# Kernel tuning notes

Measured on AMD Instinct MI355X. Metric: run time of the kernel, lower is better.

Reference implementation:

```python
import jax, jax.numpy as jnp
import numpy as np

NF4_LUT = jnp.array([-1.0, -0.6961928009986877, -0.5250730514526367, -0.39491748809814453,
                     -0.28444138169288635, -0.18477343022823334, -0.09105003625154495, 0.0,
                     0.07958029955625534, 0.16093020141124725, 0.24611230194568634,
                     0.33791524171829224, 0.44070982933044434, 0.5626170039176941,
                     0.7229568362236023, 1.0], dtype=jnp.float32)

B, S, IN, OUT, GS = 4, 2048, 4096, 4096, 128


def setup_inputs() -> dict:
    key = jax.random.key(0)
    k1, k2, k3, k4 = jax.random.split(key, 4)
    x = jax.random.normal(k1, (B, S, IN), dtype=jnp.float32)
    # each int32 entry is one packed byte holding two 4-bit NF4 codes (low nibble first)
    qweight = jax.random.randint(k2, (OUT, IN // 2), 0, 256, dtype=jnp.int32)
    scales = jax.random.uniform(k3, (OUT, IN // GS), dtype=jnp.float32, minval=0.01, maxval=0.1)
    bias = jax.random.normal(k4, (OUT,), dtype=jnp.float32)
    g_idx = (jnp.arange(IN, dtype=jnp.int32) // GS).astype(jnp.int32)
    lut = NF4_LUT
    return {"x": x, "qweight": qweight, "scales": scales, "bias": bias,
            "g_idx": g_idx, "lut": lut}


def reference(x, qweight, scales, bias, g_idx, lut):
    out_f, half_in = qweight.shape
    # unpack two 4-bit codes per byte, low nibble first (matches little-endian uint32 pack)
    low = qweight & 0xF
    high = (qweight >> 4) & 0xF
    codes = jnp.stack([low, high], axis=-1).reshape(out_f, half_in * 2)  # [OUT, IN]
    # NF4 dequant: lut lookup * per-group scale (scales gathered via g_idx)
    w = lut[codes] * scales[:, g_idx]  # [OUT, IN] float32
    y = jnp.einsum('bsi,oi->bso', x, w) + bias
    return y
```

## Files before the change

### kernel.cpp

```cpp
#include <hip/hip_runtime.h>
#include <hip/hip_bf16.h>
#include <stdint.h>

#define M_DIM 8192
#define K_DIM 4096
#define N_DIM 4096
#define NPIECE (K_DIM / 32)

#define DQ_BLOCKS 8192
#define CVT_BLOCKS 16384

typedef __bf16 bf16x8v __attribute__((ext_vector_type(8)));
typedef float f32x4 __attribute__((ext_vector_type(4)));

__device__ __forceinline__ unsigned short f2bf(float f) {
    unsigned int u = __builtin_bit_cast(unsigned int, f);
    u += 0x7FFFu + ((u >> 16) & 1u);
    return (unsigned short)(u >> 16);
}

__global__ void k_prep(const int4* __restrict__ qw4,
                       const float* __restrict__ scales,
                       const float* __restrict__ lut,
                       uint4* __restrict__ wb4,
                       const float4* __restrict__ x4,
                       uint4* __restrict__ xb4) {
    if (blockIdx.x < DQ_BLOCKS) {
        __shared__ float sl[16];
        if (threadIdx.x < 16) sl[threadIdx.x] = lut[threadIdx.x];
        __syncthreads();
        int t = blockIdx.x * blockDim.x + threadIdx.x;
        int4 q = qw4[t];
        int o = t >> 9;
        int col0 = (t & 511) << 3;
        float s = scales[(o << 5) + (col0 >> 7)];
        int v[4] = {q.x, q.y, q.z, q.w};
        unsigned int pk[4];
#pragma unroll
        for (int j = 0; j < 4; ++j) {
            float w0 = sl[v[j] & 15] * s;
            float w1 = sl[(v[j] >> 4) & 15] * s;
            pk[j] = (unsigned int)f2bf(w0) | ((unsigned int)f2bf(w1) << 16);
        }
        uint4 rr; rr.x = pk[0]; rr.y = pk[1]; rr.z = pk[2]; rr.w = pk[3];
        wb4[t] = rr;
    } else {
        int t = (blockIdx.x - DQ_BLOCKS) * blockDim.x + threadIdx.x;
        float4 a = x4[2 * t], b = x4[2 * t + 1];
        uint4 o;
        o.x = (unsigned int)f2bf(a.x) | ((unsigned int)f2bf(a.y) << 16);
        o.y = (unsigned int)f2bf(a.z) | ((unsigned int)f2bf(a.w) << 16);
        o.z = (unsigned int)f2bf(b.x) | ((unsigned int)f2bf(b.y) << 16);
        o.w = (unsigned int)f2bf(b.z) | ((unsigned int)f2bf(b.w) << 16);
        xb4[t] = o;
    }
}

#define GLL16(SRC, DST)                                                              \
    __builtin_amdgcn_global_load_lds((__attribute__((address_space(1))) void*)(SRC), \
                                     (__attribute__((address_space(3))) void*)(DST), \
                                     16, 0, 0)

__global__ __launch_bounds__(512, 2) void k_gemm(const __hip_bfloat16* __restrict__ A,
                                                 const __hip_bfloat16* __restrict__ Bw,
                                                 const float* __restrict__ bias,
                                                 float* __restrict__ C) {
    __shared__ __align__(16) char lds[4][32768];

    const int tid  = threadIdx.x;
    const int lane = tid & 63;
    const int wave = tid >> 6;
    const int wm = wave >> 2;
    const int wn = wave & 3;
    const int bm = blockIdx.y, bn = blockIdx.x;

    f32x4 acc[8][4];
    const f32x4 z = {0.f, 0.f, 0.f, 0.f};
#pragma unroll
    for (int i = 0; i < 8; ++i)
#pragma unroll
        for (int j = 0; j < 4; ++j) acc[i][j] = z;

    const int trow = tid >> 2;
    const int sg   = (tid & 3) ^ ((trow >> 1) & 3);
    const char* aSrc = (const char*)A  + ((size_t)(bm * 256 + trow) * K_DIM) * 2 + sg * 16;
    const char* bSrc = (const char*)Bw + ((size_t)(bn * 256 + trow) * K_DIM) * 2 + sg * 16;
    const size_t hop = (size_t)128 * K_DIM * 2;
    const int woff = wave * 1024;

    const int r   = lane & 15;
    const int kq  = lane >> 4;
    const int gsw = kq ^ ((r >> 1) & 3);
    const int aOff = (wm * 128 + r) * 64 + gsw * 16;
    const int bOff = 16384 + (wn * 64 + r) * 64 + gsw * 16;

    const int gc0 = bn * 256 + wn * 64 + r;
    float bv[4];
#pragma unroll
    for (int n = 0; n < 4; ++n) bv[n] = bias[gc0 + n * 16];

    bf16x8v aC[4], aN[4], bX[4], bY[4];

#define STAGE_A(P)                                                           \
    do {                                                                     \
        char* d_ = (char*)lds[(P) & 3];                                      \
        const size_t ko_ = (size_t)(P) * 64;                                 \
        GLL16(aSrc + ko_,       d_ + 0    + woff);                           \
        GLL16(aSrc + hop + ko_, d_ + 8192 + woff);                           \
    } while (0)
#define STAGE_B(P)                                                           \
    do {                                                                     \
        char* d_ = (char*)lds[(P) & 3];                                      \
        const size_t ko_ = (size_t)(P) * 64;                                 \
        GLL16(bSrc + ko_,       d_ + 16384 + woff);                          \
        GLL16(bSrc + hop + ko_, d_ + 24576 + woff);                          \
    } while (0)

#define PIECE_BODY(P, BCUR, BNXT, GLLON, RDNEXT, WAITSTR)                                              \
    do {                                                                                               \
        const char* slC_ = (const char*)&lds[0][0] + (((P) & 3) << 15);                                \
        const char* slN_ = (const char*)&lds[0][0] + ((((P) + 1) & 3) << 15);                          \
                         \
        if (GLLON) { STAGE_A((P) + 3); STAGE_B((P) + 3); }                                             \
        _Pragma("unroll") for (int m = 0; m < 4; ++m)                                                  \
            aN[m] = *(const bf16x8v*)(slC_ + aOff + (m + 4) * 1024);                                   \
        asm volatile("" ::: "memory");                                                                 \
        __builtin_amdgcn_s_setprio(1);                                                                 \
        _Pragma("unroll") for (int m = 0; m < 4; ++m)                                                  \
            _Pragma("unroll") for (int n = 0; n < 4; ++n)                                              \
                acc[m][n] = __builtin_amdgcn_mfma_f32_16x16x32_bf16(aC[m], BCUR[n], acc[m][n], 0, 0, 0); \
        __builtin_amdgcn_s_setprio(0);                                                                 \
                                          \
        if (RDNEXT) {                                                                                  \
            _Pragma("unroll") for (int m = 0; m < 4; ++m)                                              \
                aC[m] = *(const bf16x8v*)(slN_ + aOff + m * 1024);                                     \
            _Pragma("unroll") for (int n = 0; n < 4; ++n)                                              \
                BNXT[n] = *(const bf16x8v*)(slN_ + bOff + n * 1024);                                   \
        }                                                                                              \
        asm volatile("" ::: "memory");                                                                 \
        __builtin_amdgcn_s_setprio(1);                                                                 \
        _Pragma("unroll") for (int m = 0; m < 4; ++m)                                                  \
            _Pragma("unroll") for (int n = 0; n < 4; ++n)                                              \
                acc[m + 4][n] =                                                                        \
                    __builtin_amdgcn_mfma_f32_16x16x32_bf16(aN[m], BCUR[n], acc[m + 4][n], 0, 0, 0);   \
        __builtin_amdgcn_s_setprio(0);                                                                 \
        asm volatile(WAITSTR ::: "memory");                                                            \
        __builtin_amdgcn_s_barrier();                                                                  \
        asm volatile("" ::: "memory");                                                                 \
    } while (0)

    STAGE_A(0); STAGE_B(0);
    STAGE_A(1); STAGE_B(1);
    STAGE_A(2); STAGE_B(2);
    asm volatile("s_waitcnt vmcnt(4)" ::: "memory");
    __builtin_amdgcn_s_barrier();
    asm volatile("" ::: "memory");
#pragma unroll
    for (int m = 0; m < 4; ++m)
        aC[m] = *(const bf16x8v*)((const char*)&lds[0][0] + aOff + m * 1024);
#pragma unroll
    for (int n = 0; n < 4; ++n)
        bX[n] = *(const bf16x8v*)((const char*)&lds[0][0] + bOff + n * 1024);

    for (int p = 0; p < NPIECE - 4; p += 2) {
        PIECE_BODY(p,     bX, bY, 1, 1, "s_waitcnt vmcnt(4)");
        PIECE_BODY(p + 1, bY, bX, 1, 1, "s_waitcnt vmcnt(4)");
    }
    PIECE_BODY(124, bX, bY, 1, 1, "s_waitcnt vmcnt(4)");
    PIECE_BODY(125, bY, bX, 0, 1, "s_waitcnt vmcnt(0)");
    PIECE_BODY(126, bX, bY, 0, 1, "s_nop 0");
    PIECE_BODY(127, bY, bX, 0, 0, "s_nop 0");

#undef PIECE_BODY
#undef STAGE_A
#undef STAGE_B

    const int q   = lane >> 4;
    const int gr0 = bm * 256 + wm * 128;
#pragma unroll
    for (int m = 0; m < 8; ++m)
#pragma unroll
        for (int j = 0; j < 4; ++j) {
            float* crow = C + (size_t)(gr0 + m * 16 + q * 4 + j) * N_DIM + gc0;
#pragma unroll
            for (int n = 0; n < 4; ++n)
                crow[n * 16] = acc[m][n][j] + bv[n];
        }
}

__global__ void k_naive(const float* __restrict__ x, const int* __restrict__ qw,
                        const float* __restrict__ scales, const float* __restrict__ bias,
                        const float* __restrict__ lut, float* __restrict__ y) {
    long t = (long)blockIdx.x * blockDim.x + threadIdx.x;
    if (t >= (long)M_DIM * N_DIM) return;
    int m = (int)(t / N_DIM), n = (int)(t % N_DIM);
    float acc = 0.f;
    for (int k = 0; k < K_DIM; k += 2) {
        int b = qw[n * (K_DIM / 2) + (k >> 1)];
        float s = scales[n * 32 + (k >> 7)];
        acc += x[(size_t)m * K_DIM + k]     * lut[b & 15]        * s;
        acc += x[(size_t)m * K_DIM + k + 1] * lut[(b >> 4) & 15] * s;
    }
    y[t] = acc + bias[n];
}

extern "C" void kernel_launch(void* const* d_in, const int* in_sizes, int n_in,
                              void* d_out, int out_size, void* d_ws, size_t ws_size,
                              hipStream_t stream) {
    const float* x      = (const float*)d_in[0];
    const int*   qw     = (const int*)d_in[1];
    const float* scales = (const float*)d_in[2];
    const float* bias   = (const float*)d_in[3];
    const float* lut    = (const float*)d_in[5];
    float* y = (float*)d_out;

    const size_t wbBytes = (size_t)N_DIM * K_DIM * 2;
    const size_t xbBytes = (size_t)M_DIM * K_DIM * 2;
    if (ws_size < wbBytes + xbBytes) {
        long total = (long)M_DIM * N_DIM;
        k_naive<<<(int)((total + 255) / 256), 256, 0, stream>>>(x, qw, scales, bias, lut, y);
        return;
    }
    __hip_bfloat16* Wb = (__hip_bfloat16*)d_ws;
    __hip_bfloat16* Xb = (__hip_bfloat16*)((char*)d_ws + wbBytes);

    k_prep<<<DQ_BLOCKS + CVT_BLOCKS, 256, 0, stream>>>(
        (const int4*)qw, scales, lut, (uint4*)Wb, (const float4*)x, (uint4*)Xb);
    dim3 grid(N_DIM / 256, M_DIM / 256);
    k_gemm<<<grid, 512, 0, stream>>>(Xb, Wb, bias, y);
}
```

Measured before the change: 288.7 us.

## Use five-slot LDS ring and barrier once per two K-pieces

Grows the GEMM shared-memory ring from four to five 32 KB slots so a block-wide wait and barrier is needed only after every pair of K pieces instead of after every piece. Global-to-LDS prefetch issue moves after the first A fragment reads, the bias load moves to the epilogue, and launch bounds drop to one block per CU to leave the compiler more registers. The trade-off is that each sync now drains all outstanding loads, including one issued only a piece earlier, so less prefetch latency may be hidden, and the larger LDS footprint caps residency at one block.

```diff
diff --git a/kernel.cpp b/kernel.cpp
--- a/kernel.cpp
+++ b/kernel.cpp
@@ -61,11 +61,11 @@
                                      (__attribute__((address_space(3))) void*)(DST), \
                                      16, 0, 0)
 
-__global__ __launch_bounds__(512, 2) void k_gemm(const __hip_bfloat16* __restrict__ A,
+__global__ __launch_bounds__(512, 1) void k_gemm(const __hip_bfloat16* __restrict__ A,
                                                  const __hip_bfloat16* __restrict__ Bw,
                                                  const float* __restrict__ bias,
                                                  float* __restrict__ C) {
-    __shared__ __align__(16) char lds[4][32768];
+    __shared__ __align__(16) char lds[5][32768];
 
     const int tid  = threadIdx.x;
     const int lane = tid & 63;
@@ -94,43 +94,41 @@
     const int aOff = (wm * 128 + r) * 64 + gsw * 16;
     const int bOff = 16384 + (wn * 64 + r) * 64 + gsw * 16;
 
-    const int gc0 = bn * 256 + wn * 64 + r;
-    float bv[4];
-#pragma unroll
-    for (int n = 0; n < 4; ++n) bv[n] = bias[gc0 + n * 16];
-
     bf16x8v aC[4], aN[4], bX[4], bY[4];
+
+#define SLOT(P) ((const char*)&lds[0][0] + (size_t)((P) % 5) * 32768)
+#define SLOTW(P) ((char*)&lds[0][0] + (size_t)((P) % 5) * 32768)
 
 #define STAGE_A(P)                                                           \
     do {                                                                     \
-        char* d_ = (char*)lds[(P) & 3];                                      \
+        char* d_ = SLOTW(P);                                                 \
         const size_t ko_ = (size_t)(P) * 64;                                 \
         GLL16(aSrc + ko_,       d_ + 0    + woff);                           \
         GLL16(aSrc + hop + ko_, d_ + 8192 + woff);                           \
     } while (0)
 #define STAGE_B(P)                                                           \
     do {                                                                     \
-        char* d_ = (char*)lds[(P) & 3];                                      \
+        char* d_ = SLOTW(P);                                                 \
         const size_t ko_ = (size_t)(P) * 64;                                 \
         GLL16(bSrc + ko_,       d_ + 16384 + woff);                          \
         GLL16(bSrc + hop + ko_, d_ + 24576 + woff);                          \
     } while (0)
 
-#define PIECE_BODY(P, BCUR, BNXT, GLLON, RDNEXT, WAITSTR)                                              \
+#define PIECE_CORE(P, BCUR, BNXT, GLLON, RDNEXT)                                                       \
     do {                                                                                               \
-        const char* slC_ = (const char*)&lds[0][0] + (((P) & 3) << 15);                                \
-        const char* slN_ = (const char*)&lds[0][0] + ((((P) + 1) & 3) << 15);                          \
-                         \
-        if (GLLON) { STAGE_A((P) + 3); STAGE_B((P) + 3); }                                             \
+        const char* slC_ = SLOT(P);                                                                    \
+        const char* slN_ = SLOT((P) + 1);                                                              \
+                                   \
         _Pragma("unroll") for (int m = 0; m < 4; ++m)                                                  \
             aN[m] = *(const bf16x8v*)(slC_ + aOff + (m + 4) * 1024);                                   \
+        if (GLLON) { STAGE_A((P) + 3); STAGE_B((P) + 3); }                                             \
         asm volatile("" ::: "memory");                                                                 \
         __builtin_amdgcn_s_setprio(1);                                                                 \
         _Pragma("unroll") for (int m = 0; m < 4; ++m)                                                  \
             _Pragma("unroll") for (int n = 0; n < 4; ++n)                                              \
                 acc[m][n] = __builtin_amdgcn_mfma_f32_16x16x32_bf16(aC[m], BCUR[n], acc[m][n], 0, 0, 0); \
         __builtin_amdgcn_s_setprio(0);                                                                 \
-                                          \
+                                                \
         if (RDNEXT) {                                                                                  \
             _Pragma("unroll") for (int m = 0; m < 4; ++m)                                              \
                 aC[m] = *(const bf16x8v*)(slN_ + aOff + m * 1024);                                     \
@@ -144,17 +142,19 @@
                 acc[m + 4][n] =                                                                        \
                     __builtin_amdgcn_mfma_f32_16x16x32_bf16(aN[m], BCUR[n], acc[m + 4][n], 0, 0, 0);   \
         __builtin_amdgcn_s_setprio(0);                                                                 \
-        asm volatile(WAITSTR ::: "memory");                                                            \
-        __builtin_amdgcn_s_barrier();                                                                  \
-        asm volatile("" ::: "memory");                                                                 \
+    } while (0)
+
+#define SYNC(WAITSTR)                                                        \
+    do {                                                                     \
+        asm volatile(WAITSTR ::: "memory");                                  \
+        __builtin_amdgcn_s_barrier();                                        \
+        asm volatile("" ::: "memory");                                       \
     } while (0)
 
     STAGE_A(0); STAGE_B(0);
     STAGE_A(1); STAGE_B(1);
     STAGE_A(2); STAGE_B(2);
-    asm volatile("s_waitcnt vmcnt(4)" ::: "memory");
-    __builtin_amdgcn_s_barrier();
-    asm volatile("" ::: "memory");
+    SYNC("s_waitcnt vmcnt(0)");
 #pragma unroll
     for (int m = 0; m < 4; ++m)
         aC[m] = *(const bf16x8v*)((const char*)&lds[0][0] + aOff + m * 1024);
@@ -163,20 +163,29 @@
         bX[n] = *(const bf16x8v*)((const char*)&lds[0][0] + bOff + n * 1024);
 
     for (int p = 0; p < NPIECE - 4; p += 2) {
-        PIECE_BODY(p,     bX, bY, 1, 1, "s_waitcnt vmcnt(4)");
-        PIECE_BODY(p + 1, bY, bX, 1, 1, "s_waitcnt vmcnt(4)");
-    }
-    PIECE_BODY(124, bX, bY, 1, 1, "s_waitcnt vmcnt(4)");
-    PIECE_BODY(125, bY, bX, 0, 1, "s_waitcnt vmcnt(0)");
-    PIECE_BODY(126, bX, bY, 0, 1, "s_nop 0");
-    PIECE_BODY(127, bY, bX, 0, 0, "s_nop 0");
-
-#undef PIECE_BODY
+        PIECE_CORE(p,     bX, bY, 1, 1);
+        PIECE_CORE(p + 1, bY, bX, 1, 1);
+        SYNC("s_waitcnt vmcnt(0)");
+    }
+    PIECE_CORE(124, bX, bY, 1, 1);
+    PIECE_CORE(125, bY, bX, 0, 1);
+    SYNC("s_waitcnt vmcnt(0)");
+    PIECE_CORE(126, bX, bY, 0, 1);
+    PIECE_CORE(127, bY, bX, 0, 0);
+
+#undef PIECE_CORE
+#undef SYNC
 #undef STAGE_A
 #undef STAGE_B
+#undef SLOT
+#undef SLOTW
 
     const int q   = lane >> 4;
     const int gr0 = bm * 256 + wm * 128;
+    const int gc0 = bn * 256 + wn * 64 + r;
+    float bv[4];
+#pragma unroll
+    for (int n = 0; n < 4; ++n) bv[n] = bias[gc0 + n * 16];
 #pragma unroll
     for (int m = 0; m < 8; ++m)
 #pragma unroll
```

New measurement: 290.7 us. Within noise of the previous version (+0.7%).
